# Optimization experiments

Measured on AMD Instinct MI355X. Metric: run time of the kernel, lower is better.

## Reference

```python
import jax, jax.numpy as jnp
import numpy as np

E = 1024      # d_model
H = 16        # num heads
D = E // H    # head dim = 64
FF = 4096     # dim_feedforward
WIN = 128
EPS = 1e-5    # layer-norm eps
NEG = -1e9


def setup_inputs() -> dict:
    key = jax.random.key(0)
    ks = jax.random.split(key, 16)
    s = 0.02
    f32 = jnp.float32
    return {
        "src":       jax.random.normal(ks[0], (2, 2048, E), f32),
        "in_proj_w": jax.random.normal(ks[1], (3 * E, E), f32) * s,
        "in_proj_b": jnp.zeros((3 * E,), f32),
        "out_w":     jax.random.normal(ks[2], (E, E), f32) * s,
        "out_b":     jnp.zeros((E,), f32),
        "lin1_w":    jax.random.normal(ks[3], (FF, E), f32) * s,
        "lin1_b":    jnp.zeros((FF,), f32),
        "lin2_w":    jax.random.normal(ks[4], (E, FF), f32) * s,
        "lin2_b":    jnp.zeros((E,), f32),
        "ln1_g":     jnp.ones((E,), f32),
        "ln1_beta":  jnp.zeros((E,), f32),
        "ln2_g":     jnp.ones((E,), f32),
        "ln2_beta":  jnp.zeros((E,), f32),
    }


def _layer_norm(x, g, b):
    mu = x.mean(-1, keepdims=True)
    var = ((x - mu) ** 2).mean(-1, keepdims=True)
    return (x - mu) * jax.lax.rsqrt(var + EPS) * g + b


def reference(src, in_proj_w, in_proj_b, out_w, out_b,
              lin1_w, lin1_b, lin2_w, lin2_b,
              ln1_g, ln1_beta, ln2_g, ln2_beta):
    B, L, _ = src.shape  # batch_first=True
    x = src

    # fused QKV projection (torch Linear: y = x @ W.T + b)
    qkv = x @ in_proj_w.T + in_proj_b            # [B, L, 3E]
    q, k, v = jnp.split(qkv, 3, axis=-1)
    q = q.reshape(B, L, H, D)
    k = k.reshape(B, L, H, D)
    v = v.reshape(B, L, H, D)

    scores = jnp.einsum('blhd,bmhd->bhlm', q, k) / np.float32(np.sqrt(D))
    idx = jnp.arange(L)
    band = jnp.abs(idx[:, None] - idx[None, :]) <= WIN   # [L, L] allowed positions
    scores = jnp.where(band, scores, NEG)
    attn = jax.nn.softmax(scores, axis=-1)

    ctx = jnp.einsum('bhlm,bmhd->blhd', attn, v).reshape(B, L, E)
    attn_out = ctx @ out_w.T + out_b

    # post-norm transformer encoder layer (norm_first=False default)
    x = _layer_norm(x + attn_out, ln1_g, ln1_beta)
    ff = jax.nn.relu(x @ lin1_w.T + lin1_b) @ lin2_w.T + lin2_b
    return _layer_norm(x + ff, ln2_g, ln2_beta)
```

## Files before the change

kernel.cpp:

```cpp
#include <hip/hip_runtime.h>
#include <cstdint>
#include <cstddef>


typedef __attribute__((ext_vector_type(8))) short short8;
typedef __attribute__((ext_vector_type(4))) float f32x4;

__device__ __forceinline__ float b2f(unsigned short u) {
  union { unsigned int i; float f; } x; x.i = ((unsigned int)u) << 16; return x.f;
}
__device__ __forceinline__ unsigned short f2b(float f) {
  union { float f; unsigned int i; } x; x.f = f;
  unsigned int i = x.i;
  unsigned int r = (i + 0x7FFFu + ((i >> 16) & 1u)) >> 16;
  return (unsigned short)r;
}
__device__ __forceinline__ uint4 pack8(float4 f0, float4 f1) {
  uint4 r;
  r.x = (unsigned)f2b(f0.x) | ((unsigned)f2b(f0.y) << 16);
  r.y = (unsigned)f2b(f0.z) | ((unsigned)f2b(f0.w) << 16);
  r.z = (unsigned)f2b(f1.x) | ((unsigned)f2b(f1.y) << 16);
  r.w = (unsigned)f2b(f1.z) | ((unsigned)f2b(f1.w) << 16);
  return r;
}

__device__ __forceinline__ void gl_lds16(const unsigned short* g, unsigned short* l) {
  __builtin_amdgcn_global_load_lds(
      (const __attribute__((address_space(1))) unsigned int*)g,
      (__attribute__((address_space(3))) unsigned int*)l, 16, 0, 0);
}

__global__ __launch_bounds__(256) void conv_k(
    const float* __restrict__ in, unsigned short* __restrict__ out, int n)
{
  const int i = (blockIdx.x * 256 + threadIdx.x) * 8;
  if (i < n) {
    const float4 f0 = *(const float4*)(in + i);
    const float4 f1 = *(const float4*)(in + i + 4);
    *(uint4*)(out + i) = pack8(f0, f1);
  }
}

template<int RELU, int OUT32>
__global__ __launch_bounds__(512, 2) void gemm256(
    const unsigned short* __restrict__ A, const unsigned short* __restrict__ Wb,
    const float* __restrict__ bias, void* __restrict__ out,
    int M, int N, int K)
{
  __shared__ unsigned short As[2][256 * 64];
  __shared__ unsigned short Bs[2][256 * 64];

  const int tid = threadIdx.x;
  const int lane = tid & 63, wid = tid >> 6;
  const int wm = wid >> 2, wn = wid & 3;

  const int gx = gridDim.x;
  const int flat = blockIdx.y * gx + blockIdx.x;
  const int chunk = (gx * gridDim.y) >> 3;
  const int nf = (flat & 7) * chunk + (flat >> 3);
  const int m0 = (nf / gx) * 256, n0 = (nf % gx) * 256;

  const unsigned short* gA[4];
  const unsigned short* gW[4];
  int ldsO[4];
#pragma unroll
  for (int i = 0; i < 4; ++i) {
    const int sbase = i * 512 + (tid & ~63);
    const int sl = sbase + lane;
    const int r = sl >> 3, s = sl & 7, c = (s + r) & 7;
    gA[i] = A + (size_t)(m0 + r) * K + c * 8;
    gW[i] = Wb + (size_t)(n0 + r) * K + c * 8;
    ldsO[i] = sbase * 8;
  }

  const int cl = lane & 15;
  const int kg = lane >> 4;

  f32x4 acc[8][4];
#pragma unroll
  for (int i = 0; i < 8; ++i)
#pragma unroll
    for (int j = 0; j < 4; ++j) acc[i][j] = (f32x4){0.f, 0.f, 0.f, 0.f};

  const int steps = K >> 6;

  const int pre = steps < 2 ? steps : 2;
  for (int t = 0; t < pre; ++t) {
#pragma unroll
    for (int i = 0; i < 4; ++i) { gl_lds16(gA[i], &As[t][ldsO[i]]); gA[i] += 64; }
#pragma unroll
    for (int i = 0; i < 4; ++i) { gl_lds16(gW[i], &Bs[t][ldsO[i]]); gW[i] += 64; }
  }

  int cur = 0;
  for (int s = 0; s < steps; ++s) {
    if (s + 1 < steps) asm volatile("s_waitcnt vmcnt(8)" ::: "memory");
    else               asm volatile("s_waitcnt vmcnt(0)" ::: "memory");
    __builtin_amdgcn_s_barrier();

    short8 bf[4][2];
#pragma unroll
    for (int nt = 0; nt < 4; ++nt)
#pragma unroll
      for (int ks = 0; ks < 2; ++ks) {
        const int br = wn * 64 + nt * 16 + cl;
        bf[nt][ks] = *(const short8*)&Bs[cur][br * 64 + (((ks * 4 + kg) - br) & 7) * 8];
      }
    short8 af[4][2];
#pragma unroll
    for (int mt = 0; mt < 4; ++mt)
#pragma unroll
      for (int ks = 0; ks < 2; ++ks) {
        const int ar = wm * 128 + mt * 16 + cl;
        af[mt][ks] = *(const short8*)&As[cur][ar * 64 + (((ks * 4 + kg) - ar) & 7) * 8];
      }

    __builtin_amdgcn_s_setprio(1);
#pragma unroll
    for (int mt = 0; mt < 4; ++mt)
#pragma unroll
      for (int nt = 0; nt < 4; ++nt)
#pragma unroll
        for (int ks = 0; ks < 2; ++ks)
          acc[mt][nt] = __builtin_amdgcn_mfma_f32_16x16x32_bf16(af[mt][ks], bf[nt][ks], acc[mt][nt], 0, 0, 0);
    __builtin_amdgcn_s_setprio(0);

    short8 ag[4][2];
#pragma unroll
    for (int mt = 0; mt < 4; ++mt)
#pragma unroll
      for (int ks = 0; ks < 2; ++ks) {
        const int ar = wm * 128 + (mt + 4) * 16 + cl;
        ag[mt][ks] = *(const short8*)&As[cur][ar * 64 + (((ks * 4 + kg) - ar) & 7) * 8];
      }

    asm volatile("s_waitcnt lgkmcnt(0)" ::: "memory");
    __builtin_amdgcn_sched_barrier(0);
    __builtin_amdgcn_s_barrier();

    if (s + 2 < steps) {
#pragma unroll
      for (int i = 0; i < 4; ++i) { gl_lds16(gA[i], &As[cur][ldsO[i]]); gA[i] += 64; }
#pragma unroll
      for (int i = 0; i < 4; ++i) { gl_lds16(gW[i], &Bs[cur][ldsO[i]]); gW[i] += 64; }
    }

    __builtin_amdgcn_s_setprio(1);
#pragma unroll
    for (int mt = 0; mt < 4; ++mt)
#pragma unroll
      for (int nt = 0; nt < 4; ++nt)
#pragma unroll
        for (int ks = 0; ks < 2; ++ks)
          acc[mt + 4][nt] = __builtin_amdgcn_mfma_f32_16x16x32_bf16(ag[mt][ks], bf[nt][ks], acc[mt + 4][nt], 0, 0, 0);
    __builtin_amdgcn_s_setprio(0);

    cur ^= 1;
  }

#pragma unroll
  for (int nt = 0; nt < 4; ++nt) {
    const int col = n0 + wn * 64 + nt * 16 + cl;
    const float bvs = bias[col];
#pragma unroll
    for (int mt = 0; mt < 8; ++mt) {
#pragma unroll
      for (int r = 0; r < 4; ++r) {
        const int grow = m0 + wm * 128 + mt * 16 + kg * 4 + r;
        float v = acc[mt][nt][r] + bvs;
        if (RELU) v = fmaxf(v, 0.f);
        if (OUT32) ((float*)out)[(size_t)grow * N + col] = v;
        else       ((unsigned short*)out)[(size_t)grow * N + col] = f2b(v);
      }
    }
  }
}

template<int OUT32>
__global__ __launch_bounds__(256) void gemm64(
    const unsigned short* __restrict__ A, const unsigned short* __restrict__ Wb,
    const float* __restrict__ bias, void* __restrict__ out,
    int M, int N, int K)
{
  __shared__ unsigned short As[3][64 * 64];
  __shared__ unsigned short Bs[3][128 * 64];

  const int tid = threadIdx.x;
  const int lane = tid & 63, wid = tid >> 6;

  const int nwgx = gridDim.x;
  const int flat = blockIdx.y * nwgx + blockIdx.x;
  const int chunk = (nwgx * gridDim.y) >> 3;
  const int nf = (flat & 7) * chunk + (flat >> 3);
  const int m0 = (nf / nwgx) * 64, n0 = (nf % nwgx) * 128;

  const unsigned short* gA[2];
  const unsigned short* gW[4];
  int ldsA[2], ldsB[4];
#pragma unroll
  for (int i = 0; i < 2; ++i) {
    const int sl = wid * 128 + i * 64 + lane;
    const int r = sl >> 3, s = sl & 7, c = (s + r) & 7;
    gA[i] = A + (size_t)(m0 + r) * K + c * 8;
    ldsA[i] = (wid * 128 + i * 64) * 8;
  }
#pragma unroll
  for (int i = 0; i < 4; ++i) {
    const int sl = wid * 256 + i * 64 + lane;
    const int r = sl >> 3, s = sl & 7, c = (s + r) & 7;
    gW[i] = Wb + (size_t)(n0 + r) * K + c * 8;
    ldsB[i] = (wid * 256 + i * 64) * 8;
  }

  const int cl = lane & 15;
  const int kg = lane >> 4;
  int aoff[4][2], boff[2][2];
#pragma unroll
  for (int t = 0; t < 4; ++t) {
    const int ar = t * 16 + cl;
#pragma unroll
    for (int ks = 0; ks < 2; ++ks)
      aoff[t][ks] = ar * 64 + ((ks * 4 + kg - ar) & 7) * 8;
  }
#pragma unroll
  for (int t = 0; t < 2; ++t) {
    const int br = wid * 32 + t * 16 + cl;
#pragma unroll
    for (int ks = 0; ks < 2; ++ks)
      boff[t][ks] = br * 64 + ((ks * 4 + kg - br) & 7) * 8;
  }

  f32x4 acc[4][2];
#pragma unroll
  for (int i = 0; i < 4; ++i)
#pragma unroll
    for (int j = 0; j < 2; ++j) acc[i][j] = (f32x4){0.f, 0.f, 0.f, 0.f};

  const int steps = K >> 6;

  const int pre = steps < 3 ? steps : 3;
  for (int t = 0; t < pre; ++t) {
#pragma unroll
    for (int i = 0; i < 2; ++i) { gl_lds16(gA[i], &As[t][ldsA[i]]); gA[i] += 64; }
#pragma unroll
    for (int i = 0; i < 4; ++i) { gl_lds16(gW[i], &Bs[t][ldsB[i]]); gW[i] += 64; }
  }

  int cur = 0;
  for (int s = 0; s < steps; ++s) {
    const int rem = steps - 1 - s;
    if (rem >= 2)      asm volatile("s_waitcnt vmcnt(12)" ::: "memory");
    else if (rem == 1) asm volatile("s_waitcnt vmcnt(6)" ::: "memory");
    else               asm volatile("s_waitcnt vmcnt(0)" ::: "memory");
    __builtin_amdgcn_s_barrier();

    short8 af[4][2], bf[2][2];
#pragma unroll
    for (int t = 0; t < 4; ++t)
#pragma unroll
      for (int ks = 0; ks < 2; ++ks) af[t][ks] = *(const short8*)&As[cur][aoff[t][ks]];
#pragma unroll
    for (int t = 0; t < 2; ++t)
#pragma unroll
      for (int ks = 0; ks < 2; ++ks) bf[t][ks] = *(const short8*)&Bs[cur][boff[t][ks]];

    asm volatile("s_waitcnt lgkmcnt(0)" ::: "memory");
    __builtin_amdgcn_sched_barrier(0);
    __builtin_amdgcn_s_barrier();

    if (s + 3 < steps) {
#pragma unroll
      for (int i = 0; i < 2; ++i) { gl_lds16(gA[i], &As[cur][ldsA[i]]); gA[i] += 64; }
#pragma unroll
      for (int i = 0; i < 4; ++i) { gl_lds16(gW[i], &Bs[cur][ldsB[i]]); gW[i] += 64; }
    }

#pragma unroll
    for (int mt = 0; mt < 4; ++mt)
#pragma unroll
      for (int nt = 0; nt < 2; ++nt)
#pragma unroll
        for (int ks = 0; ks < 2; ++ks)
          acc[mt][nt] = __builtin_amdgcn_mfma_f32_16x16x32_bf16(af[mt][ks], bf[nt][ks], acc[mt][nt], 0, 0, 0);

    cur = (cur == 2) ? 0 : cur + 1;
  }

#pragma unroll
  for (int nt = 0; nt < 2; ++nt) {
    const int col = n0 + wid * 32 + nt * 16 + cl;
    const float bvs = bias[col];
#pragma unroll
    for (int mt = 0; mt < 4; ++mt) {
#pragma unroll
      for (int r = 0; r < 4; ++r) {
        const int grow = m0 + mt * 16 + kg * 4 + r;
        const float v = acc[mt][nt][r] + bvs;
        if (OUT32) ((float*)out)[(size_t)grow * N + col] = v;
        else       ((unsigned short*)out)[(size_t)grow * N + col] = f2b(v);
      }
    }
  }
}

__global__ __launch_bounds__(256) void attn_mfma(
    const unsigned short* __restrict__ qkv, unsigned short* __restrict__ ctx)
{
  __shared__ unsigned short Ks[64 * 72];
  __shared__ unsigned short Vt[64 * 72];
  __shared__ unsigned short Ps[64 * 72];

  const int tid = threadIdx.x;
  const int bid = blockIdx.x;
  const int qt = bid & 31, h = (bid >> 5) & 15, b = bid >> 9;
  const int q0 = qt * 64;
  const int wstart = max(0, q0 - 128);
  const int wend = min(2048, q0 + 64 + 128);
  const int ntile = (wend - wstart + 63) >> 6;
  const size_t rowb = (size_t)b * 2048;

  const int lane = tid & 63, wid = tid >> 6;
  const int cl = lane & 15;
  const int kq = (lane >> 4) * 8;
  const int rowg = lane >> 4;

  short8 aQ[2];
#pragma unroll
  for (int ks = 0; ks < 2; ++ks)
    aQ[ks] = *(const short8*)(qkv + (rowb + q0 + wid * 16 + cl) * 3072 + h * 64 + ks * 32 + kq);

  float m_i[4], l_i[4];
  f32x4 O[4];
#pragma unroll
  for (int r = 0; r < 4; ++r) { m_i[r] = -1.0e30f; l_i[r] = 0.f; }
#pragma unroll
  for (int nt = 0; nt < 4; ++nt) O[nt] = (f32x4){0.f, 0.f, 0.f, 0.f};

  for (int t = 0; t < ntile; ++t) {
    const int jbase = wstart + t * 64;
    __syncthreads();
    for (int idx = tid; idx < 512; idx += 256) {
      const int r = idx >> 3, c = idx & 7;
      const int jg = jbase + r;
      uint4 kv = {0u, 0u, 0u, 0u}, vv = {0u, 0u, 0u, 0u};
      if (jg < wend) {
        const size_t base = (rowb + jg) * 3072 + h * 64 + c * 8;
        kv = *(const uint4*)(qkv + base + 1024);
        vv = *(const uint4*)(qkv + base + 2048);
      }
      *(uint4*)&Ks[r * 72 + c * 8] = kv;
      const unsigned short* vs = (const unsigned short*)&vv;
#pragma unroll
      for (int ii = 0; ii < 8; ++ii) Vt[(c * 8 + ii) * 72 + r] = vs[ii];
    }
    __syncthreads();

    f32x4 S[4];
#pragma unroll
    for (int nt = 0; nt < 4; ++nt) S[nt] = (f32x4){0.f, 0.f, 0.f, 0.f};
#pragma unroll
    for (int nt = 0; nt < 4; ++nt)
#pragma unroll
      for (int ks = 0; ks < 2; ++ks) {
        const short8 bK = *(const short8*)&Ks[(nt * 16 + cl) * 72 + ks * 32 + kq];
        S[nt] = __builtin_amdgcn_mfma_f32_16x16x32_bf16(aQ[ks], bK, S[nt], 0, 0, 0);
      }

    float sc[4][4];
#pragma unroll
    for (int nt = 0; nt < 4; ++nt) {
      const int jg = jbase + nt * 16 + cl;
#pragma unroll
      for (int r = 0; r < 4; ++r) {
        const int i = q0 + wid * 16 + rowg * 4 + r;
        const bool v = (jg < wend) && (jg >= i - 128) && (jg <= i + 128);
        sc[nt][r] = v ? S[nt][r] * 0.125f : -1.0e30f;
      }
    }

    float alpha[4], p[4][4];
#pragma unroll
    for (int r = 0; r < 4; ++r) {
      float tm = fmaxf(fmaxf(sc[0][r], sc[1][r]), fmaxf(sc[2][r], sc[3][r]));
      tm = fmaxf(tm, __shfl_xor(tm, 1, 64));
      tm = fmaxf(tm, __shfl_xor(tm, 2, 64));
      tm = fmaxf(tm, __shfl_xor(tm, 4, 64));
      tm = fmaxf(tm, __shfl_xor(tm, 8, 64));
      const float mn = fmaxf(m_i[r], tm);
      alpha[r] = __expf(m_i[r] - mn);
      m_i[r] = mn;
      float ps = 0.f;
#pragma unroll
      for (int nt = 0; nt < 4; ++nt) { p[nt][r] = __expf(sc[nt][r] - mn); ps += p[nt][r]; }
      ps += __shfl_xor(ps, 1, 64);
      ps += __shfl_xor(ps, 2, 64);
      ps += __shfl_xor(ps, 4, 64);
      ps += __shfl_xor(ps, 8, 64);
      l_i[r] = l_i[r] * alpha[r] + ps;
    }

#pragma unroll
    for (int nt = 0; nt < 4; ++nt)
#pragma unroll
      for (int r = 0; r < 4; ++r)
        Ps[(wid * 16 + rowg * 4 + r) * 72 + nt * 16 + cl] = f2b(p[nt][r]);
    __syncthreads();

#pragma unroll
    for (int nt = 0; nt < 4; ++nt)
#pragma unroll
      for (int r = 0; r < 4; ++r) O[nt][r] *= alpha[r];
    short8 aP[2];
#pragma unroll
    for (int ks = 0; ks < 2; ++ks)
      aP[ks] = *(const short8*)&Ps[(wid * 16 + cl) * 72 + ks * 32 + kq];
#pragma unroll
    for (int nt = 0; nt < 4; ++nt)
#pragma unroll
      for (int ks = 0; ks < 2; ++ks) {
        const short8 bV = *(const short8*)&Vt[(nt * 16 + cl) * 72 + ks * 32 + kq];
        O[nt] = __builtin_amdgcn_mfma_f32_16x16x32_bf16(aP[ks], bV, O[nt], 0, 0, 0);
      }
  }

#pragma unroll
  for (int nt = 0; nt < 4; ++nt) {
    const int d = nt * 16 + cl;
#pragma unroll
    for (int r = 0; r < 4; ++r) {
      const int i = q0 + wid * 16 + rowg * 4 + r;
      ctx[(rowb + i) * 1024 + h * 64 + d] = f2b(O[nt][r] / l_i[r]);
    }
  }
}

template<int AF32, int BF32, int OF32>
__global__ __launch_bounds__(256) void ln_k(
    const void* __restrict__ a, const void* __restrict__ b,
    const float* __restrict__ g, const float* __restrict__ be,
    void* __restrict__ o)
{
  __shared__ float rbuf[8];
  const int tid = threadIdx.x;
  const size_t base = (size_t)blockIdx.x * 1024;
  const int lane = tid & 63, wid = tid >> 6;

  float xv[4], s = 0.f, sq = 0.f;
#pragma unroll
  for (int t = 0; t < 4; ++t) {
    const int c = tid + t * 256;
    const float av = AF32 ? ((const float*)a)[base + c]
                          : b2f(((const unsigned short*)a)[base + c]);
    const float bv = BF32 ? ((const float*)b)[base + c]
                          : b2f(((const unsigned short*)b)[base + c]);
    const float x = av + bv;
    xv[t] = x; s += x; sq += x * x;
  }
  for (int o2 = 1; o2 < 64; o2 <<= 1) { s += __shfl_xor(s, o2, 64); sq += __shfl_xor(sq, o2, 64); }
  if (lane == 0) { rbuf[wid] = s; rbuf[wid + 4] = sq; }
  __syncthreads();
  s  = rbuf[0] + rbuf[1] + rbuf[2] + rbuf[3];
  sq = rbuf[4] + rbuf[5] + rbuf[6] + rbuf[7];
  const float mean = s * (1.0f / 1024.f);
  const float var = sq * (1.0f / 1024.f) - mean * mean;
  const float rstd = rsqrtf(var + 1e-5f);
#pragma unroll
  for (int t = 0; t < 4; ++t) {
    const int c = tid + t * 256;
    const float y = (xv[t] - mean) * rstd * g[c] + be[c];
    if (OF32) ((float*)o)[base + c] = y;
    else      ((unsigned short*)o)[base + c] = f2b(y);
  }
}

extern "C" void kernel_launch(void* const* d_in, const int* in_sizes, int n_in,
                              void* d_out, int out_size, void* d_ws, size_t ws_size,
                              hipStream_t stream)
{
  (void)in_sizes; (void)n_in; (void)out_size; (void)ws_size;
  const float* src   = (const float*)d_in[0];
  const float* w_in  = (const float*)d_in[1];
  const float* b_in  = (const float*)d_in[2];
  const float* w_out = (const float*)d_in[3];
  const float* b_out = (const float*)d_in[4];
  const float* w1    = (const float*)d_in[5];
  const float* b1    = (const float*)d_in[6];
  const float* w2    = (const float*)d_in[7];
  const float* b2    = (const float*)d_in[8];
  const float* g1    = (const float*)d_in[9];
  const float* be1   = (const float*)d_in[10];
  const float* g2    = (const float*)d_in[11];
  const float* be2   = (const float*)d_in[12];

  char* ws = (char*)d_ws;
  unsigned short* srcb  = (unsigned short*)(ws);
  unsigned short* x1b   = srcb;
  unsigned short* qkv   = (unsigned short*)(ws + 8388608);
  unsigned short* ctx   = (unsigned short*)(ws + 33554432);
  unsigned short* attnb = (unsigned short*)(ws + 8388608);
  unsigned short* ff1   = (unsigned short*)(ws + 8388608);
  unsigned short* wslot = (unsigned short*)(ws + 41943040);
  float*          outf  = (float*)d_out;

  conv_k<<<dim3(2048), 256, 0, stream>>>(src, srcb, 4194304);
  conv_k<<<dim3(1536), 256, 0, stream>>>(w_in, wslot, 3145728);
  gemm256<0, 0><<<dim3(12, 16), 512, 0, stream>>>(srcb, wslot, b_in, qkv, 4096, 3072, 1024);
  attn_mfma<<<dim3(1024), 256, 0, stream>>>(qkv, ctx);
  conv_k<<<dim3(512), 256, 0, stream>>>(w_out, wslot, 1048576);
  gemm64<0><<<dim3(8, 64), 256, 0, stream>>>(ctx, wslot, b_out, attnb, 4096, 1024, 1024);
  ln_k<0, 0, 0><<<dim3(4096), 256, 0, stream>>>(srcb, attnb, g1, be1, x1b);
  conv_k<<<dim3(2048), 256, 0, stream>>>(w1, wslot, 4194304);
  gemm256<1, 0><<<dim3(16, 16), 512, 0, stream>>>(x1b, wslot, b1, ff1, 4096, 4096, 1024);
  conv_k<<<dim3(2048), 256, 0, stream>>>(w2, wslot, 4194304);
  gemm64<1><<<dim3(8, 64), 256, 0, stream>>>(ff1, wslot, b2, outf, 4096, 1024, 4096);
  ln_k<0, 1, 1><<<dim3(4096), 256, 0, stream>>>(x1b, outf, g2, be2, outf);
}
```

Baseline: 312.0 us.

## Merge weight conversions into one launch and widen gemm64 per-warp tiles

Three fp32-to-bf16 conversion launches (src, in_proj weight, out_proj weight) become one kernel, with the out_proj weight placed after the in_proj weight in the slot. gemm64 now runs 2 waves of 128 threads instead of 4, each wave computing a 64x64 sub-tile instead of 64x32. The loaded A fragments are reused across twice as many MFMAs, and fewer LDS reads happen per MFMA. In exchange each wave holds more accumulator registers, and the 512-block grid now has half as many waves to hide latency.

```diff
diff --git a/kernel.cpp b/kernel.cpp
--- a/kernel.cpp
+++ b/kernel.cpp
@@ -41,6 +41,22 @@
   }
 }
 
+__global__ __launch_bounds__(256) void conv3_k(
+    const float* __restrict__ src, unsigned short* __restrict__ srcb,
+    const float* __restrict__ w_in, const float* __restrict__ w_out,
+    unsigned short* __restrict__ wslot)
+{
+  const int i = (blockIdx.x * 256 + threadIdx.x) * 8;
+  const float* in;
+  unsigned short* out;
+  if (i < 4194304)      { in = src + i;                 out = srcb + i; }
+  else if (i < 7340032) { in = w_in + (i - 4194304);    out = wslot + (i - 4194304); }
+  else                  { in = w_out + (i - 7340032);   out = wslot + (i - 4194304); }
+  const float4 f0 = *(const float4*)(in);
+  const float4 f1 = *(const float4*)(in + 4);
+  *(uint4*)(out) = pack8(f0, f1);
+}
+
 template<int RELU, int OUT32>
 __global__ __launch_bounds__(512, 2) void gemm256(
     const unsigned short* __restrict__ A, const unsigned short* __restrict__ Wb,
@@ -177,7 +193,7 @@
 }
 
 template<int OUT32>
-__global__ __launch_bounds__(256) void gemm64(
+__global__ __launch_bounds__(128) void gemm64(
     const unsigned short* __restrict__ A, const unsigned short* __restrict__ Wb,
     const float* __restrict__ bias, void* __restrict__ out,
     int M, int N, int K)
@@ -194,75 +210,70 @@
   const int nf = (flat & 7) * chunk + (flat >> 3);
   const int m0 = (nf / nwgx) * 64, n0 = (nf % nwgx) * 128;
 
-  const unsigned short* gA[2];
-  const unsigned short* gW[4];
-  int ldsA[2], ldsB[4];
-#pragma unroll
-  for (int i = 0; i < 2; ++i) {
-    const int sl = wid * 128 + i * 64 + lane;
+  const unsigned short* gA[4];
+  const unsigned short* gW[8];
+  int ldsA[4], ldsB[8];
+#pragma unroll
+  for (int i = 0; i < 4; ++i) {
+    const int sl = i * 128 + tid;
     const int r = sl >> 3, s = sl & 7, c = (s + r) & 7;
     gA[i] = A + (size_t)(m0 + r) * K + c * 8;
-    ldsA[i] = (wid * 128 + i * 64) * 8;
-  }
-#pragma unroll
-  for (int i = 0; i < 4; ++i) {
-    const int sl = wid * 256 + i * 64 + lane;
+    ldsA[i] = (i * 128 + wid * 64) * 8;
+  }
+#pragma unroll
+  for (int i = 0; i < 8; ++i) {
+    const int sl = i * 128 + tid;
     const int r = sl >> 3, s = sl & 7, c = (s + r) & 7;
     gW[i] = Wb + (size_t)(n0 + r) * K + c * 8;
-    ldsB[i] = (wid * 256 + i * 64) * 8;
+    ldsB[i] = (i * 128 + wid * 64) * 8;
   }
 
   const int cl = lane & 15;
   const int kg = lane >> 4;
-  int aoff[4][2], boff[2][2];
+  int aoff[4][2], boff[4][2];
 #pragma unroll
   for (int t = 0; t < 4; ++t) {
     const int ar = t * 16 + cl;
-#pragma unroll
-    for (int ks = 0; ks < 2; ++ks)
+    const int br = wid * 64 + t * 16 + cl;
+#pragma unroll
+    for (int ks = 0; ks < 2; ++ks) {
       aoff[t][ks] = ar * 64 + ((ks * 4 + kg - ar) & 7) * 8;
-  }
-#pragma unroll
-  for (int t = 0; t < 2; ++t) {
-    const int br = wid * 32 + t * 16 + cl;
-#pragma unroll
-    for (int ks = 0; ks < 2; ++ks)
       boff[t][ks] = br * 64 + ((ks * 4 + kg - br) & 7) * 8;
-  }
-
-  f32x4 acc[4][2];
+    }
+  }
+
+  f32x4 acc[4][4];
 #pragma unroll
   for (int i = 0; i < 4; ++i)
 #pragma unroll
-    for (int j = 0; j < 2; ++j) acc[i][j] = (f32x4){0.f, 0.f, 0.f, 0.f};
+    for (int j = 0; j < 4; ++j) acc[i][j] = (f32x4){0.f, 0.f, 0.f, 0.f};
 
   const int steps = K >> 6;
 
   const int pre = steps < 3 ? steps : 3;
   for (int t = 0; t < pre; ++t) {
 #pragma unroll
-    for (int i = 0; i < 2; ++i) { gl_lds16(gA[i], &As[t][ldsA[i]]); gA[i] += 64; }
-#pragma unroll
-    for (int i = 0; i < 4; ++i) { gl_lds16(gW[i], &Bs[t][ldsB[i]]); gW[i] += 64; }
+    for (int i = 0; i < 4; ++i) { gl_lds16(gA[i], &As[t][ldsA[i]]); gA[i] += 64; }
+#pragma unroll
+    for (int i = 0; i < 8; ++i) { gl_lds16(gW[i], &Bs[t][ldsB[i]]); gW[i] += 64; }
   }
 
   int cur = 0;
   for (int s = 0; s < steps; ++s) {
     const int rem = steps - 1 - s;
-    if (rem >= 2)      asm volatile("s_waitcnt vmcnt(12)" ::: "memory");
-    else if (rem == 1) asm volatile("s_waitcnt vmcnt(6)" ::: "memory");
+    if (rem >= 2)      asm volatile("s_waitcnt vmcnt(24)" ::: "memory");
+    else if (rem == 1) asm volatile("s_waitcnt vmcnt(12)" ::: "memory");
     else               asm volatile("s_waitcnt vmcnt(0)" ::: "memory");
     __builtin_amdgcn_s_barrier();
 
-    short8 af[4][2], bf[2][2];
+    short8 af[4][2], bf[4][2];
 #pragma unroll
     for (int t = 0; t < 4; ++t)
 #pragma unroll
-      for (int ks = 0; ks < 2; ++ks) af[t][ks] = *(const short8*)&As[cur][aoff[t][ks]];
-#pragma unroll
-    for (int t = 0; t < 2; ++t)
-#pragma unroll
-      for (int ks = 0; ks < 2; ++ks) bf[t][ks] = *(const short8*)&Bs[cur][boff[t][ks]];
+      for (int ks = 0; ks < 2; ++ks) {
+        af[t][ks] = *(const short8*)&As[cur][aoff[t][ks]];
+        bf[t][ks] = *(const short8*)&Bs[cur][boff[t][ks]];
+      }
 
     asm volatile("s_waitcnt lgkmcnt(0)" ::: "memory");
     __builtin_amdgcn_sched_barrier(0);
@@ -270,15 +281,15 @@
 
     if (s + 3 < steps) {
 #pragma unroll
-      for (int i = 0; i < 2; ++i) { gl_lds16(gA[i], &As[cur][ldsA[i]]); gA[i] += 64; }
-#pragma unroll
-      for (int i = 0; i < 4; ++i) { gl_lds16(gW[i], &Bs[cur][ldsB[i]]); gW[i] += 64; }
+      for (int i = 0; i < 4; ++i) { gl_lds16(gA[i], &As[cur][ldsA[i]]); gA[i] += 64; }
+#pragma unroll
+      for (int i = 0; i < 8; ++i) { gl_lds16(gW[i], &Bs[cur][ldsB[i]]); gW[i] += 64; }
     }
 
 #pragma unroll
     for (int mt = 0; mt < 4; ++mt)
 #pragma unroll
-      for (int nt = 0; nt < 2; ++nt)
+      for (int nt = 0; nt < 4; ++nt)
 #pragma unroll
         for (int ks = 0; ks < 2; ++ks)
           acc[mt][nt] = __builtin_amdgcn_mfma_f32_16x16x32_bf16(af[mt][ks], bf[nt][ks], acc[mt][nt], 0, 0, 0);
@@ -287,8 +298,8 @@
   }
 
 #pragma unroll
-  for (int nt = 0; nt < 2; ++nt) {
-    const int col = n0 + wid * 32 + nt * 16 + cl;
+  for (int nt = 0; nt < 4; ++nt) {
+    const int col = n0 + wid * 64 + nt * 16 + cl;
     const float bvs = bias[col];
 #pragma unroll
     for (int mt = 0; mt < 4; ++mt) {
@@ -502,16 +513,14 @@
   unsigned short* wslot = (unsigned short*)(ws + 41943040);
   float*          outf  = (float*)d_out;
 
-  conv_k<<<dim3(2048), 256, 0, stream>>>(src, srcb, 4194304);
-  conv_k<<<dim3(1536), 256, 0, stream>>>(w_in, wslot, 3145728);
+  conv3_k<<<dim3(4096), 256, 0, stream>>>(src, srcb, w_in, w_out, wslot);
   gemm256<0, 0><<<dim3(12, 16), 512, 0, stream>>>(srcb, wslot, b_in, qkv, 4096, 3072, 1024);
   attn_mfma<<<dim3(1024), 256, 0, stream>>>(qkv, ctx);
-  conv_k<<<dim3(512), 256, 0, stream>>>(w_out, wslot, 1048576);
-  gemm64<0><<<dim3(8, 64), 256, 0, stream>>>(ctx, wslot, b_out, attnb, 4096, 1024, 1024);
+  gemm64<0><<<dim3(8, 64), 128, 0, stream>>>(ctx, wslot + 3145728, b_out, attnb, 4096, 1024, 1024);
   ln_k<0, 0, 0><<<dim3(4096), 256, 0, stream>>>(srcb, attnb, g1, be1, x1b);
   conv_k<<<dim3(2048), 256, 0, stream>>>(w1, wslot, 4194304);
   gemm256<1, 0><<<dim3(16, 16), 512, 0, stream>>>(x1b, wslot, b1, ff1, 4096, 4096, 1024);
   conv_k<<<dim3(2048), 256, 0, stream>>>(w2, wslot, 4194304);
-  gemm64<1><<<dim3(8, 64), 256, 0, stream>>>(ff1, wslot, b2, outf, 4096, 1024, 4096);
+  gemm64<1><<<dim3(8, 64), 128, 0, stream>>>(ff1, wslot, b2, outf, 4096, 1024, 4096);
   ln_k<0, 1, 1><<<dim3(4096), 256, 0, stream>>>(x1b, outf, g2, be2, outf);
 }
```

Measured after the change: 308.8 us. About the same (-1.0%).

## Restructure 256-tile GEMM into four-phase interleaved pipeline and merge conversion launches

Applied to the files above, without the earlier changes.

The 256x256 GEMM main loop is split into four MFMA phases over half-tiles of A and B. Global-to-LDS loads are issued in quarter-tile chunks between phases, so memory traffic overlaps compute more finely. Warp tiling now places each wave's subtiles in two 128-row and 128-column halves, with precomputed LDS offsets. Separately, the src, in-proj and out-proj fp32-to-bf16 conversions are merged into one launch, with the out-proj weights stored after the in-proj weights in the weight slot. This adds more barriers per step and tighter vmcnt bookkeeping, and the weight slot must now be large enough to hold both conversions.

```diff
diff --git a/kernel.cpp b/kernel.cpp
--- a/kernel.cpp
+++ b/kernel.cpp
@@ -41,6 +41,22 @@
   }
 }
 
+__global__ __launch_bounds__(256) void conv3_k(
+    const float* __restrict__ src, unsigned short* __restrict__ srcb,
+    const float* __restrict__ w_in, const float* __restrict__ w_out,
+    unsigned short* __restrict__ wslot)
+{
+  const int i = (blockIdx.x * 256 + threadIdx.x) * 8;
+  const float* in;
+  unsigned short* out;
+  if (i < 4194304)      { in = src + i;                 out = srcb + i; }
+  else if (i < 7340032) { in = w_in + (i - 4194304);    out = wslot + (i - 4194304); }
+  else                  { in = w_out + (i - 7340032);   out = wslot + (i - 4194304); }
+  const float4 f0 = *(const float4*)(in);
+  const float4 f1 = *(const float4*)(in + 4);
+  *(uint4*)(out) = pack8(f0, f1);
+}
+
 template<int RELU, int OUT32>
 __global__ __launch_bounds__(512, 2) void gemm256(
     const unsigned short* __restrict__ A, const unsigned short* __restrict__ Wb,
@@ -60,22 +76,39 @@
   const int nf = (flat & 7) * chunk + (flat >> 3);
   const int m0 = (nf / gx) * 256, n0 = (nf % gx) * 256;
 
-  const unsigned short* gA[4];
-  const unsigned short* gW[4];
-  int ldsO[4];
-#pragma unroll
-  for (int i = 0; i < 4; ++i) {
-    const int sbase = i * 512 + (tid & ~63);
-    const int sl = sbase + lane;
-    const int r = sl >> 3, s = sl & 7, c = (s + r) & 7;
-    gA[i] = A + (size_t)(m0 + r) * K + c * 8;
-    gW[i] = Wb + (size_t)(n0 + r) * K + c * 8;
-    ldsO[i] = sbase * 8;
-  }
+  int offA[2][2], offB[2][2], ldsO2[2][2];
+#pragma unroll
+  for (int h1 = 0; h1 < 2; ++h1)
+#pragma unroll
+    for (int i = 0; i < 2; ++i) {
+      const int sl = i * 512 + tid;
+      const int r = h1 * 128 + (sl >> 3);
+      const int sslot = sl & 7;
+      const int c = (sslot + r) & 7;
+      offA[h1][i] = (m0 + r) * K + c * 8;
+      offB[h1][i] = (n0 + r) * K + c * 8;
+      ldsO2[h1][i] = (h1 * 1024 + i * 512 + (tid & ~63)) * 8;
+    }
 
   const int cl = lane & 15;
   const int kg = lane >> 4;
 
+  int aoff[4][2], boff[2][2];
+#pragma unroll
+  for (int mt = 0; mt < 4; ++mt) {
+    const int ar = wm * 64 + mt * 16 + cl;
+#pragma unroll
+    for (int ks = 0; ks < 2; ++ks)
+      aoff[mt][ks] = ar * 64 + (((ks * 4 + kg) - ar) & 7) * 8;
+  }
+#pragma unroll
+  for (int nt = 0; nt < 2; ++nt) {
+    const int br = wn * 32 + nt * 16 + cl;
+#pragma unroll
+    for (int ks = 0; ks < 2; ++ks)
+      boff[nt][ks] = br * 64 + (((ks * 4 + kg) - br) & 7) * 8;
+  }
+
   f32x4 acc[8][4];
 #pragma unroll
   for (int i = 0; i < 8; ++i)
@@ -84,89 +117,120 @@
 
   const int steps = K >> 6;
 
-  const int pre = steps < 2 ? steps : 2;
-  for (int t = 0; t < pre; ++t) {
-#pragma unroll
-    for (int i = 0; i < 4; ++i) { gl_lds16(gA[i], &As[t][ldsO[i]]); gA[i] += 64; }
-#pragma unroll
-    for (int i = 0; i < 4; ++i) { gl_lds16(gW[i], &Bs[t][ldsO[i]]); gW[i] += 64; }
-  }
+#define STAGE256(idx_) do { const int _x = (idx_); if (_x < 4 * steps) {        \
+    const int T_ = _x >> 2, j_ = _x & 3, bf_ = T_ & 1; const int ko = T_ << 6;  \
+    if (j_ == 0)      { gl_lds16(A  + offA[0][0] + ko, &As[bf_][ldsO2[0][0]]);  \
+                        gl_lds16(A  + offA[0][1] + ko, &As[bf_][ldsO2[0][1]]); }\
+    else if (j_ == 1) { gl_lds16(Wb + offB[0][0] + ko, &Bs[bf_][ldsO2[0][0]]);  \
+                        gl_lds16(Wb + offB[0][1] + ko, &Bs[bf_][ldsO2[0][1]]); }\
+    else if (j_ == 2) { gl_lds16(Wb + offB[1][0] + ko, &Bs[bf_][ldsO2[1][0]]);  \
+                        gl_lds16(Wb + offB[1][1] + ko, &Bs[bf_][ldsO2[1][1]]); }\
+    else              { gl_lds16(A  + offA[1][0] + ko, &As[bf_][ldsO2[1][0]]);  \
+                        gl_lds16(A  + offA[1][1] + ko, &As[bf_][ldsO2[1][1]]); }\
+  } } while (0)
+
+  STAGE256(0); STAGE256(1); STAGE256(2); STAGE256(3);
+  STAGE256(4); STAGE256(5); STAGE256(6);
+  asm volatile("s_waitcnt vmcnt(6)" ::: "memory");
+  __builtin_amdgcn_s_barrier();
 
   int cur = 0;
   for (int s = 0; s < steps; ++s) {
-    if (s + 1 < steps) asm volatile("s_waitcnt vmcnt(8)" ::: "memory");
-    else               asm volatile("s_waitcnt vmcnt(0)" ::: "memory");
-    __builtin_amdgcn_s_barrier();
-
-    short8 bf[4][2];
-#pragma unroll
-    for (int nt = 0; nt < 4; ++nt)
-#pragma unroll
-      for (int ks = 0; ks < 2; ++ks) {
-        const int br = wn * 64 + nt * 16 + cl;
-        bf[nt][ks] = *(const short8*)&Bs[cur][br * 64 + (((ks * 4 + kg) - br) & 7) * 8];
-      }
-    short8 af[4][2];
-#pragma unroll
-    for (int mt = 0; mt < 4; ++mt)
-#pragma unroll
-      for (int ks = 0; ks < 2; ++ks) {
-        const int ar = wm * 128 + mt * 16 + cl;
-        af[mt][ks] = *(const short8*)&As[cur][ar * 64 + (((ks * 4 + kg) - ar) & 7) * 8];
-      }
-
-    __builtin_amdgcn_s_setprio(1);
-#pragma unroll
-    for (int mt = 0; mt < 4; ++mt)
-#pragma unroll
-      for (int nt = 0; nt < 4; ++nt)
-#pragma unroll
-        for (int ks = 0; ks < 2; ++ks)
-          acc[mt][nt] = __builtin_amdgcn_mfma_f32_16x16x32_bf16(af[mt][ks], bf[nt][ks], acc[mt][nt], 0, 0, 0);
-    __builtin_amdgcn_s_setprio(0);
-
-    short8 ag[4][2];
-#pragma unroll
-    for (int mt = 0; mt < 4; ++mt)
-#pragma unroll
-      for (int ks = 0; ks < 2; ++ks) {
-        const int ar = wm * 128 + (mt + 4) * 16 + cl;
-        ag[mt][ks] = *(const short8*)&As[cur][ar * 64 + (((ks * 4 + kg) - ar) & 7) * 8];
-      }
-
+    short8 bf0[2][2], af[4][2];
+#pragma unroll
+    for (int nt = 0; nt < 2; ++nt)
+#pragma unroll
+      for (int ks = 0; ks < 2; ++ks) bf0[nt][ks] = *(const short8*)&Bs[cur][boff[nt][ks]];
+#pragma unroll
+    for (int mt = 0; mt < 4; ++mt)
+#pragma unroll
+      for (int ks = 0; ks < 2; ++ks) af[mt][ks] = *(const short8*)&As[cur][aoff[mt][ks]];
+    STAGE256(4 * s + 7);
+    asm volatile("s_waitcnt lgkmcnt(8)" ::: "memory");
+    __builtin_amdgcn_s_barrier();
     asm volatile("s_waitcnt lgkmcnt(0)" ::: "memory");
     __builtin_amdgcn_sched_barrier(0);
-    __builtin_amdgcn_s_barrier();
-
-    if (s + 2 < steps) {
-#pragma unroll
-      for (int i = 0; i < 4; ++i) { gl_lds16(gA[i], &As[cur][ldsO[i]]); gA[i] += 64; }
-#pragma unroll
-      for (int i = 0; i < 4; ++i) { gl_lds16(gW[i], &Bs[cur][ldsO[i]]); gW[i] += 64; }
-    }
-
     __builtin_amdgcn_s_setprio(1);
 #pragma unroll
     for (int mt = 0; mt < 4; ++mt)
 #pragma unroll
-      for (int nt = 0; nt < 4; ++nt)
+      for (int nt = 0; nt < 2; ++nt)
 #pragma unroll
         for (int ks = 0; ks < 2; ++ks)
-          acc[mt + 4][nt] = __builtin_amdgcn_mfma_f32_16x16x32_bf16(ag[mt][ks], bf[nt][ks], acc[mt + 4][nt], 0, 0, 0);
+          acc[mt][nt] = __builtin_amdgcn_mfma_f32_16x16x32_bf16(af[mt][ks], bf0[nt][ks], acc[mt][nt], 0, 0, 0);
     __builtin_amdgcn_s_setprio(0);
+    __builtin_amdgcn_s_barrier();
+
+    short8 bf1[2][2];
+#pragma unroll
+    for (int nt = 0; nt < 2; ++nt)
+#pragma unroll
+      for (int ks = 0; ks < 2; ++ks) bf1[nt][ks] = *(const short8*)&Bs[cur][boff[nt][ks] + 8192];
+    STAGE256(4 * s + 8);
+    __builtin_amdgcn_s_barrier();
+    asm volatile("s_waitcnt lgkmcnt(0)" ::: "memory");
+    __builtin_amdgcn_sched_barrier(0);
+    __builtin_amdgcn_s_setprio(1);
+#pragma unroll
+    for (int mt = 0; mt < 4; ++mt)
+#pragma unroll
+      for (int nt = 0; nt < 2; ++nt)
+#pragma unroll
+        for (int ks = 0; ks < 2; ++ks)
+          acc[mt][nt + 2] = __builtin_amdgcn_mfma_f32_16x16x32_bf16(af[mt][ks], bf1[nt][ks], acc[mt][nt + 2], 0, 0, 0);
+    __builtin_amdgcn_s_setprio(0);
+    __builtin_amdgcn_s_barrier();
+
+    short8 ag[4][2];
+#pragma unroll
+    for (int mt = 0; mt < 4; ++mt)
+#pragma unroll
+      for (int ks = 0; ks < 2; ++ks) ag[mt][ks] = *(const short8*)&As[cur][aoff[mt][ks] + 8192];
+    STAGE256(4 * s + 9);
+    __builtin_amdgcn_s_barrier();
+    asm volatile("s_waitcnt lgkmcnt(0)" ::: "memory");
+    __builtin_amdgcn_sched_barrier(0);
+    __builtin_amdgcn_s_setprio(1);
+#pragma unroll
+    for (int mt = 0; mt < 4; ++mt)
+#pragma unroll
+      for (int nt = 0; nt < 2; ++nt)
+#pragma unroll
+        for (int ks = 0; ks < 2; ++ks)
+          acc[mt + 4][nt] = __builtin_amdgcn_mfma_f32_16x16x32_bf16(ag[mt][ks], bf0[nt][ks], acc[mt + 4][nt], 0, 0, 0);
+    __builtin_amdgcn_s_setprio(0);
+    __builtin_amdgcn_s_barrier();
+
+    STAGE256(4 * s + 10);
+    if (s < steps - 2)       asm volatile("s_waitcnt vmcnt(6)" ::: "memory");
+    else if (s == steps - 2) asm volatile("s_waitcnt vmcnt(0)" ::: "memory");
+    __builtin_amdgcn_s_barrier();
+    __builtin_amdgcn_s_setprio(1);
+#pragma unroll
+    for (int mt = 0; mt < 4; ++mt)
+#pragma unroll
+      for (int nt = 0; nt < 2; ++nt)
+#pragma unroll
+        for (int ks = 0; ks < 2; ++ks)
+          acc[mt + 4][nt + 2] = __builtin_amdgcn_mfma_f32_16x16x32_bf16(ag[mt][ks], bf1[nt][ks], acc[mt + 4][nt + 2], 0, 0, 0);
+    __builtin_amdgcn_s_setprio(0);
+    __builtin_amdgcn_s_barrier();
 
     cur ^= 1;
   }
+#undef STAGE256
 
 #pragma unroll
   for (int nt = 0; nt < 4; ++nt) {
-    const int col = n0 + wn * 64 + nt * 16 + cl;
+    const int colB = wn * 32 + (nt & 1) * 16 + (nt >> 1) * 128;
+    const int col = n0 + colB + cl;
     const float bvs = bias[col];
 #pragma unroll
     for (int mt = 0; mt < 8; ++mt) {
+      const int rowA = wm * 64 + (mt & 3) * 16 + (mt >> 2) * 128;
 #pragma unroll
       for (int r = 0; r < 4; ++r) {
-        const int grow = m0 + wm * 128 + mt * 16 + kg * 4 + r;
+        const int grow = m0 + rowA + kg * 4 + r;
         float v = acc[mt][nt][r] + bvs;
         if (RELU) v = fmaxf(v, 0.f);
         if (OUT32) ((float*)out)[(size_t)grow * N + col] = v;
@@ -502,12 +566,10 @@
   unsigned short* wslot = (unsigned short*)(ws + 41943040);
   float*          outf  = (float*)d_out;
 
-  conv_k<<<dim3(2048), 256, 0, stream>>>(src, srcb, 4194304);
-  conv_k<<<dim3(1536), 256, 0, stream>>>(w_in, wslot, 3145728);
+  conv3_k<<<dim3(4096), 256, 0, stream>>>(src, srcb, w_in, w_out, wslot);
   gemm256<0, 0><<<dim3(12, 16), 512, 0, stream>>>(srcb, wslot, b_in, qkv, 4096, 3072, 1024);
   attn_mfma<<<dim3(1024), 256, 0, stream>>>(qkv, ctx);
-  conv_k<<<dim3(512), 256, 0, stream>>>(w_out, wslot, 1048576);
-  gemm64<0><<<dim3(8, 64), 256, 0, stream>>>(ctx, wslot, b_out, attnb, 4096, 1024, 1024);
+  gemm64<0><<<dim3(8, 64), 256, 0, stream>>>(ctx, wslot + 3145728, b_out, attnb, 4096, 1024, 1024);
   ln_k<0, 0, 0><<<dim3(4096), 256, 0, stream>>>(srcb, attnb, g1, be1, x1b);
   conv_k<<<dim3(2048), 256, 0, stream>>>(w1, wslot, 4194304);
   gemm256<1, 0><<<dim3(16, 16), 512, 0, stream>>>(x1b, wslot, b1, ff1, 4096, 4096, 1024);
```

After: 305.9 us. No clear change (-1.9%).
